# Kernel tuning notes

Measured on AMD Instinct MI355X. Metric: run time of the kernel, lower is better.

## Reference

```python
import jax, jax.numpy as jnp
import numpy as np

B, S, D = 4, 2048, 1024
H = 16
DH = D // H
MLP_DIM = 4096
EPS = 1e-6


def setup_inputs() -> dict:
    key = jax.random.key(0)
    ks = jax.random.split(key, 16)
    sd = lambda fi, fo: (1.0 / np.sqrt(fi))
    return {
        "x": jax.random.normal(ks[0], (B, S, D), jnp.float32),
        "Wq": jax.random.normal(ks[1], (D, D), jnp.float32) * sd(D, D),
        "bq": jnp.zeros((D,), jnp.float32),
        "Wk": jax.random.normal(ks[2], (D, D), jnp.float32) * sd(D, D),
        "bk": jnp.zeros((D,), jnp.float32),
        "Wv": jax.random.normal(ks[3], (D, D), jnp.float32) * sd(D, D),
        "bv": jnp.zeros((D,), jnp.float32),
        "Wo": jax.random.normal(ks[4], (D, D), jnp.float32) * sd(D, D),
        "bo": jnp.zeros((D,), jnp.float32),
        "ln1_g": jnp.ones((D,), jnp.float32),
        "ln1_b": jnp.zeros((D,), jnp.float32),
        "ln2_g": jnp.ones((D,), jnp.float32),
        "ln2_b": jnp.zeros((D,), jnp.float32),
        "W1": jax.random.normal(ks[5], (D, MLP_DIM), jnp.float32) * sd(D, MLP_DIM),
        "b1": jax.random.normal(ks[6], (MLP_DIM,), jnp.float32) * 1e-6,
        "W2": jax.random.normal(ks[7], (MLP_DIM, D), jnp.float32) * sd(MLP_DIM, D),
        "b2": jax.random.normal(ks[8], (D,), jnp.float32) * 1e-6,
    }


def _layernorm(x, g, b):
    mu = jnp.mean(x, axis=-1, keepdims=True)
    var = jnp.mean(jnp.square(x - mu), axis=-1, keepdims=True)
    return (x - mu) * jax.lax.rsqrt(var + EPS) * g + b


def reference(x, Wq, bq, Wk, bk, Wv, bv, Wo, bo,
              ln1_g, ln1_b, ln2_g, ln2_b, W1, b1, W2, b2):
    h = x
    xn = _layernorm(x, ln1_g, ln1_b)
    # Q/K/V: [B,S,D] -> [B,H,S,DH]
    def split_heads(t):
        return t.reshape(B, S, H, DH).transpose(0, 2, 1, 3)
    Q = split_heads(xn @ Wq + bq)
    K = split_heads(xn @ Wk + bk)
    V = split_heads(xn @ Wv + bv)
    scores = jnp.einsum("bhqd,bhkd->bhqk", Q, K) / np.sqrt(DH).astype(np.float32)
    a = jax.nn.softmax(scores, axis=-1)
    r = jnp.einsum("bhqk,bhkd->bhqd", a, V)          # [B,H,S,DH]
    r = r.transpose(0, 2, 1, 3).reshape(B, S, D)      # merge heads
    r = r @ Wo + bo
    x = r + h
    h = x
    xn = _layernorm(x, ln2_g, ln2_b)
    m = jax.nn.gelu(xn @ W1 + b1, approximate=False)
    m = m @ W2 + b2
    return m + h
```

## Files before the change

kernel.cpp:

```cpp
#include <hip/hip_runtime.h>
#include <math.h>

#define B_ 4
#define S_ 2048
#define D_ 1024
#define H_ 16
#define MLP_ 4096
#define MROWS 8192

typedef __attribute__((ext_vector_type(4))) float f32x4;
typedef __attribute__((ext_vector_type(16))) float f32x16;
typedef __attribute__((ext_vector_type(8))) __bf16 bf16x8;
typedef __attribute__((ext_vector_type(4))) __bf16 bf16x4;
typedef __attribute__((ext_vector_type(8))) unsigned short us8;
typedef unsigned short u16;
typedef unsigned int u32;

__device__ __forceinline__ void gload16(const void* g, void* l) {
    __builtin_amdgcn_global_load_lds((const __attribute__((address_space(1))) u32*)g,
                                     (__attribute__((address_space(3))) u32*)l, 16, 0, 0);
}

__device__ __forceinline__ float gelu_f(float v) {
    float p = fmaf(v * v, 0.044715f, 1.0f);
    float e = __builtin_amdgcn_exp2f(v * 2.3022089f * p);
    float r = __builtin_amdgcn_rcpf(e + 1.0f);
    return v - v * r;
}

__global__ __launch_bounds__(256) void ln_bf16_k(const float* __restrict__ x,
                                                 const float* __restrict__ g,
                                                 const float* __restrict__ b,
                                                 u16* __restrict__ y) {
    int row = blockIdx.x;
    int tid = threadIdx.x;
    const float* xr = x + (size_t)row * D_;
    f32x4 v = *(const f32x4*)(xr + tid * 4);
    float s = v.x + v.y + v.z + v.w;
    float ss = v.x * v.x + v.y * v.y + v.z * v.z + v.w * v.w;
    for (int off = 32; off > 0; off >>= 1) {
        s += __shfl_down(s, off, 64);
        ss += __shfl_down(ss, off, 64);
    }
    __shared__ float rs[4], rss[4];
    int lane = tid & 63, wid = tid >> 6;
    if (lane == 0) { rs[wid] = s; rss[wid] = ss; }
    __syncthreads();
    s = rs[0] + rs[1] + rs[2] + rs[3];
    ss = rss[0] + rss[1] + rss[2] + rss[3];
    float mu = s * (1.0f / D_);
    float var = ss * (1.0f / D_) - mu * mu;
    float inv = rsqrtf(var + 1e-6f);
    f32x4 gg = *(const f32x4*)(g + tid * 4);
    f32x4 bb = *(const f32x4*)(b + tid * 4);
    bf16x4 o = {(__bf16)((v.x - mu) * inv * gg.x + bb.x),
                (__bf16)((v.y - mu) * inv * gg.y + bb.y),
                (__bf16)((v.z - mu) * inv * gg.z + bb.z),
                (__bf16)((v.w - mu) * inv * gg.w + bb.w)};
    *(bf16x4*)(y + (size_t)row * D_ + tid * 4) = o;
}

__global__ void pack3_k(const float* __restrict__ a, const float* __restrict__ b,
                        const float* __restrict__ c, float* __restrict__ o) {
    const float* s = blockIdx.x == 0 ? a : (blockIdx.x == 1 ? b : c);
    o[blockIdx.x * 1024 + threadIdx.x] = s[threadIdx.x];
}

__global__ __launch_bounds__(256) void wtrans_k(const float* __restrict__ W,
                                                u16* __restrict__ Wt, int K, int N) {
    __shared__ float T[32][33];
    int tid = threadIdx.x;
    int k0 = blockIdx.y * 32, n0 = blockIdx.x * 32;
    int r = tid >> 3, c4 = (tid & 7) * 4;
    f32x4 v = *(const f32x4*)&W[(size_t)(k0 + r) * N + n0 + c4];
    T[r][c4 + 0] = v.x; T[r][c4 + 1] = v.y; T[r][c4 + 2] = v.z; T[r][c4 + 3] = v.w;
    __syncthreads();
    int n = tid >> 3, kk = (tid & 7) * 4;
    bf16x4 o = {(__bf16)T[kk + 0][n], (__bf16)T[kk + 1][n],
                (__bf16)T[kk + 2][n], (__bf16)T[kk + 3][n]};
    *(bf16x4*)&Wt[(size_t)(n0 + n) * K + k0 + kk] = o;
}

__device__ __forceinline__ int sigma_perm(int s) {
    return (s & 48) | (s & 3) | (((s >> 2) & 1) << 3) | (((s >> 3) & 1) << 2);
}
__global__ __launch_bounds__(256) void vtrans_k(const u16* __restrict__ QKV,
                                                u16* __restrict__ Vt) {
    __shared__ u16 T[64][80];
    int tid = threadIdx.x;
    int s0 = blockIdx.x * 64;
    int bh = blockIdx.y, b = bh >> 4, h = bh & 15;
    int r = tid >> 2, c0 = (tid & 3) * 16;
    const u16* src = QKV + (size_t)(b * S_ + s0 + r) * 3072 + 2048 + h * 64 + c0;
    us8 v0 = *(const us8*)src;
    us8 v1 = *(const us8*)(src + 8);
    *(us8*)&T[r][c0] = v0;
    *(us8*)&T[r][c0 + 8] = v1;
    __syncthreads();
    int dh = tid >> 2, s8 = (tid & 3) * 16;
    us8 o0, o1;
#pragma unroll
    for (int i = 0; i < 8; ++i) {
        o0[i] = T[sigma_perm(s8 + i)][dh];
        o1[i] = T[sigma_perm(s8 + 8 + i)][dh];
    }
    u16* dst = Vt + (size_t)(bh * 64 + dh) * S_ + s0 + s8;
    *(us8*)dst = o0;
    *(us8*)(dst + 8) = o1;
}

template <int EPI>
__global__ __launch_bounds__(256) void gemm_bf16(const u16* __restrict__ A,
                                                 const u16* __restrict__ Wt,
                                                 const float* __restrict__ bias,
                                                 const float* __restrict__ res,
                                                 void* __restrict__ Cout,
                                                 int M, int N, int K) {
    __shared__ u16 As[3][128 * 32];
    __shared__ u16 Bs[3][128 * 32];
    const int tid = threadIdx.x;
    const int lane = tid & 63;
    const int w = tid >> 6;
    const int nwg = gridDim.x * gridDim.y;
    int hw = blockIdx.x + gridDim.x * blockIdx.y;
    int lg = (hw & 7) * (nwg >> 3) + (hw >> 3);
    const int row0 = (lg / gridDim.x) * 128;
    const int col0 = (lg % gridDim.x) * 128;
    const int l15 = lane & 15, l16 = lane >> 4;
    const int wr = w >> 1, wc = w & 1;

    f32x4 acc[4][4];
#pragma unroll
    for (int i = 0; i < 4; ++i)
#pragma unroll
        for (int j = 0; j < 4; ++j) acc[i][j] = (f32x4){0.f, 0.f, 0.f, 0.f};

    const int srow = w * 32 + (lane >> 2);
    const size_t sboff = (size_t)(((lane & 3) ^ ((lane >> 3) & 3)) * 16);
    const char* Ag = (const char*)A + ((size_t)(row0 + srow) * K) * 2 + sboff;
    const char* Bg = (const char*)Wt + ((size_t)(col0 + srow) * K) * 2 + sboff;
    const size_t rstep = (size_t)16 * K * 2;
    const int woff = w * 2048;
    const int T = K >> 5;

#define STAGE(t, bi) do {                                      \
        size_t kb = (size_t)(t) << 6;                          \
        char* asw = (char*)As + (bi) * 8192 + woff;            \
        char* bsw = (char*)Bs + (bi) * 8192 + woff;            \
        gload16(Ag + kb, asw);                                 \
        gload16(Ag + kb + rstep, asw + 1024);                  \
        gload16(Bg + kb, bsw);                                 \
        gload16(Bg + kb + rstep, bsw + 1024);                  \
    } while (0)

    STAGE(0, 0);
    STAGE(1, 1);
    asm volatile("s_waitcnt vmcnt(4)" ::: "memory");
    __builtin_amdgcn_s_barrier();
    __builtin_amdgcn_sched_barrier(0);

    const int ksw = (l16 ^ ((l15 >> 1) & 3)) << 4;
    int bi = 0;
    for (int t = 0; t < T; ++t) {
        if (t + 2 < T) {
            int nb = bi + 2; if (nb >= 3) nb -= 3;
            STAGE(t + 2, nb);
        }
        const char* Ab = (const char*)As + bi * 8192;
        const char* Bb = (const char*)Bs + bi * 8192;
        bf16x8 af[4], bfr[4];
#pragma unroll
        for (int f = 0; f < 4; ++f) {
            af[f] = *(const bf16x8*)(Ab + (size_t)(wr * 64 + f * 16 + l15) * 64 + ksw);
            bfr[f] = *(const bf16x8*)(Bb + (size_t)(wc * 64 + f * 16 + l15) * 64 + ksw);
        }
        __builtin_amdgcn_s_setprio(1);
#pragma unroll
        for (int fi = 0; fi < 4; ++fi)
#pragma unroll
            for (int fj = 0; fj < 4; ++fj)
                acc[fi][fj] = __builtin_amdgcn_mfma_f32_16x16x32_bf16(af[fi], bfr[fj], acc[fi][fj], 0, 0, 0);
        __builtin_amdgcn_s_setprio(0);
        if (t + 2 < T) {
            asm volatile("s_waitcnt vmcnt(4)" ::: "memory");
        } else {
            asm volatile("s_waitcnt vmcnt(0)" ::: "memory");
        }
        __builtin_amdgcn_s_barrier();
        __builtin_amdgcn_sched_barrier(0);
        if (++bi >= 3) bi = 0;
    }
#undef STAGE

    const int rb = row0 + wr * 64 + (l16 << 2);
    const int cb = col0 + wc * 64 + l15;
#pragma unroll
    for (int fi = 0; fi < 4; ++fi)
#pragma unroll
        for (int fj = 0; fj < 4; ++fj) {
            int c = cb + fj * 16;
            float bv = bias[c];
#pragma unroll
            for (int rr = 0; rr < 4; ++rr) {
                int r = rb + fi * 16 + rr;
                float v = acc[fi][fj][rr] + bv;
                if (EPI == 1) v = gelu_f(v);
                if (EPI == 2) {
                    v += res[(size_t)r * N + c];
                    ((float*)Cout)[(size_t)r * N + c] = v;
                } else {
                    ((__bf16*)Cout)[(size_t)r * N + c] = (__bf16)v;
                }
            }
        }
}

__global__ __launch_bounds__(256) void attn_mfma(const u16* __restrict__ QKV,
                                                 const u16* __restrict__ Vt,
                                                 u16* __restrict__ O) {
    __shared__ u16 Ks[2][64 * 64];
    __shared__ u16 Vs[2][64 * 64];
    const int tid = threadIdx.x, lane = tid & 63, w = tid >> 6;
    int hw = blockIdx.x + gridDim.x * blockIdx.y;
    int lg = (hw & 7) * 128 + (hw >> 3);
    const int bh = lg >> 4, b = bh >> 4, h = bh & 15;
    const int q0 = (lg & 15) * 128;
    const int l31 = lane & 31, lh = lane >> 5;

    const u16* Qp = QKV + (size_t)(b * S_ + q0 + w * 32 + l31) * 3072 + h * 64 + lh * 8;
    bf16x8 qf[4];
    qf[0] = *(const bf16x8*)(Qp);
    qf[1] = *(const bf16x8*)(Qp + 16);
    qf[2] = *(const bf16x8*)(Qp + 32);
    qf[3] = *(const bf16x8*)(Qp + 48);

    f32x16 oacc[2];
    f32x16 lacc;
#pragma unroll
    for (int i = 0; i < 16; ++i) { oacc[0][i] = 0.f; oacc[1][i] = 0.f; lacc[i] = 0.f; }
    bf16x8 ones;
#pragma unroll
    for (int j = 0; j < 8; ++j) ones[j] = (__bf16)1.0f;

    const int sr = lane >> 3;
    const size_t soff = (size_t)(((lane & 7) ^ sr) << 4);
    const char* Kg = (const char*)QKV + ((size_t)b * S_ * 3072 + 1024 + h * 64) * 2;
    const char* Vg = (const char*)Vt + (size_t)bh * 64 * S_ * 2;
    const float C2 = 0.18033688011112f;

    const char* kp0 = Kg + (size_t)(w * 16 + sr) * 6144 + soff;
    const char* kp1 = kp0 + 8 * 6144;
    const char* vp0 = Vg + (size_t)(w * 16 + sr) * 4096 + soff;
    const char* vp1 = vp0 + 8 * 4096;
    const size_t KADV = 64 * 6144;
    const size_t VADV = 128;
    char* ksA = (char*)Ks[0] + w * 2048;
    char* ksB = (char*)Ks[1] + w * 2048;
    char* vsA = (char*)Vs[0] + w * 2048;
    char* vsB = (char*)Vs[1] + w * 2048;

    gload16(kp0, ksA); gload16(kp1, ksA + 1024);
    gload16(vp0, vsA); gload16(vp1, vsA + 1024);
    kp0 += KADV; kp1 += KADV; vp0 += VADV; vp1 += VADV;
    __syncthreads();

    for (int kt = 0; kt < S_ / 64; ++kt) {
        const int cur = kt & 1;
        if (kt < S_ / 64 - 1) {
            char* kd = cur ? ksA : ksB;
            char* vd = cur ? vsA : vsB;
            gload16(kp0, kd); gload16(kp1, kd + 1024);
            gload16(vp0, vd); gload16(vp1, vd + 1024);
            kp0 += KADV; kp1 += KADV; vp0 += VADV; vp1 += VADV;
        }

        const char* Kb_ = (const char*)Ks[cur];
        f32x16 sfr[2];
        __builtin_amdgcn_s_setprio(1);
#pragma unroll
        for (int kh = 0; kh < 2; ++kh) {
            int r = kh * 32 + l31;
            int rsw = (r & 7) << 4;
            const char* Kr = Kb_ + r * 128;
            f32x16 t;
#pragma unroll
            for (int i = 0; i < 16; ++i) t[i] = 0.f;
#pragma unroll
            for (int ds = 0; ds < 4; ++ds) {
                bf16x8 kf = *(const bf16x8*)(Kr + ((((ds * 2 + lh) << 4)) ^ rsw));
                t = __builtin_amdgcn_mfma_f32_32x32x16_bf16(kf, qf[ds], t, 0, 0, 0);
            }
            sfr[kh] = t;
        }
        __builtin_amdgcn_s_setprio(0);

        float pv0[16], pv1[16];
#pragma unroll
        for (int i = 0; i < 16; ++i) {
            pv0[i] = __builtin_amdgcn_exp2f(sfr[0][i] * C2);
            pv1[i] = __builtin_amdgcn_exp2f(sfr[1][i] * C2);
        }

        bf16x8 pf[4];
#pragma unroll
        for (int j = 0; j < 8; ++j) {
            pf[0][j] = (__bf16)pv0[j];
            pf[1][j] = (__bf16)pv0[8 + j];
            pf[2][j] = (__bf16)pv1[j];
            pf[3][j] = (__bf16)pv1[8 + j];
        }

        {
            const char* Vb_ = (const char*)Vs[cur];
            __builtin_amdgcn_s_setprio(1);
#pragma unroll
            for (int ks = 0; ks < 4; ++ks)
                lacc = __builtin_amdgcn_mfma_f32_32x32x16_bf16(ones, pf[ks], lacc, 0, 0, 0);
#pragma unroll
            for (int dh = 0; dh < 2; ++dh) {
                int r = dh * 32 + l31;
                int rsw = (r & 7) << 4;
                const char* Vr = Vb_ + r * 128;
#pragma unroll
                for (int ks = 0; ks < 4; ++ks) {
                    bf16x8 vf = *(const bf16x8*)(Vr + ((((ks * 2 + lh) << 4)) ^ rsw));
                    oacc[dh] = __builtin_amdgcn_mfma_f32_32x32x16_bf16(vf, pf[ks], oacc[dh], 0, 0, 0);
                }
            }
            __builtin_amdgcn_s_setprio(0);
        }
        __syncthreads();
    }

    float invl = 1.0f / lacc[0];
    char* Og = (char*)O + ((size_t)(b * S_ + q0 + w * 32 + l31) * 1024 + h * 64) * 2;
#pragma unroll
    for (int dh = 0; dh < 2; ++dh)
#pragma unroll
        for (int t4 = 0; t4 < 4; ++t4) {
            int db = dh * 32 + t4 * 8 + lh * 4;
            bf16x4 ov = {(__bf16)(oacc[dh][t4 * 4] * invl),
                         (__bf16)(oacc[dh][t4 * 4 + 1] * invl),
                         (__bf16)(oacc[dh][t4 * 4 + 2] * invl),
                         (__bf16)(oacc[dh][t4 * 4 + 3] * invl)};
            *(bf16x4*)(Og + db * 2) = ov;
        }
}

extern "C" void kernel_launch(void* const* d_in, const int* in_sizes, int n_in,
                              void* d_out, int out_size, void* d_ws, size_t ws_size,
                              hipStream_t stream) {
    const float* x     = (const float*)d_in[0];
    const float* Wq    = (const float*)d_in[1];
    const float* bq    = (const float*)d_in[2];
    const float* Wk    = (const float*)d_in[3];
    const float* bk    = (const float*)d_in[4];
    const float* Wv    = (const float*)d_in[5];
    const float* bv    = (const float*)d_in[6];
    const float* Wo    = (const float*)d_in[7];
    const float* bo    = (const float*)d_in[8];
    const float* ln1_g = (const float*)d_in[9];
    const float* ln1_b = (const float*)d_in[10];
    const float* ln2_g = (const float*)d_in[11];
    const float* ln2_b = (const float*)d_in[12];
    const float* W1    = (const float*)d_in[13];
    const float* b1    = (const float*)d_in[14];
    const float* W2    = (const float*)d_in[15];
    const float* b2    = (const float*)d_in[16];
    float* out = (float*)d_out;

    const size_t MB = 1ull << 20;
    char* ws = (char*)d_ws;
    u16* QKVb = (u16*)(ws + 0 * MB);
    u16* aout = (u16*)(ws + 48 * MB);
    u16* mid  = (u16*)(ws + 0 * MB);
    float* x2 = (float*)(ws + 64 * MB);
    float* bqkv = (float*)(ws + 64 * MB);
    u16* xn   = (u16*)(ws + 96 * MB);
    u16* Vt   = (u16*)(ws + 96 * MB);
    u16* xn2  = (u16*)(ws + 96 * MB);
    u16* Wqkvt = (u16*)(ws + 112 * MB);
    u16* Wot  = Wqkvt + (size_t)3072 * D_;
    u16* W1t  = (u16*)(ws + 112 * MB);
    u16* W2t  = (u16*)(ws + 120 * MB);

    wtrans_k<<<dim3(32, 32), 256, 0, stream>>>(Wq, Wqkvt, D_, D_);
    wtrans_k<<<dim3(32, 32), 256, 0, stream>>>(Wk, Wqkvt + (size_t)D_ * D_, D_, D_);
    wtrans_k<<<dim3(32, 32), 256, 0, stream>>>(Wv, Wqkvt + (size_t)2 * D_ * D_, D_, D_);
    wtrans_k<<<dim3(32, 32), 256, 0, stream>>>(Wo, Wot, D_, D_);
    wtrans_k<<<dim3(32, 128), 256, 0, stream>>>(W2, W2t, MLP_, D_);
    pack3_k<<<3, 1024, 0, stream>>>(bq, bk, bv, bqkv);

    ln_bf16_k<<<MROWS, 256, 0, stream>>>(x, ln1_g, ln1_b, xn);
    gemm_bf16<0><<<dim3(24, 64), 256, 0, stream>>>(xn, Wqkvt, bqkv, nullptr, QKVb, MROWS, 3072, D_);
    vtrans_k<<<dim3(32, 64), 256, 0, stream>>>(QKVb, Vt);
    attn_mfma<<<dim3(16, 64), 256, 0, stream>>>(QKVb, Vt, aout);
    gemm_bf16<2><<<dim3(8, 64), 256, 0, stream>>>(aout, Wot, bo, x, x2, MROWS, D_, D_);
    wtrans_k<<<dim3(128, 32), 256, 0, stream>>>(W1, W1t, D_, MLP_);
    ln_bf16_k<<<MROWS, 256, 0, stream>>>(x2, ln2_g, ln2_b, xn2);
    gemm_bf16<1><<<dim3(32, 64), 256, 0, stream>>>(xn2, W1t, b1, nullptr, mid, MROWS, MLP_, D_);
    gemm_bf16<2><<<dim3(8, 64), 256, 0, stream>>>(mid, W2t, b2, x2, (void*)out, MROWS, D_, MLP_);
}
```

Measured before the change: 427.2 us.

## Add wide 128x256 GEMM tile with triple buffering; fold softmax scale into Wq

Adds a new gemm_wide kernel that computes 128x256 output tiles with a three-stage LDS ring fed by direct global-to-LDS loads. It is used for the QKV and W1 projections, halving the grid in N and raising the reuse of each A tile. Separately, the softmax scale constant is folded into the Wq weights and bq bias during transposition, which removes a multiply per score inside attention. The wider tile uses more accumulator registers and LDS, which may lower occupancy.

After: 506.8 us. +18.6%, slower.

```diff
diff --git a/kernel.cpp b/kernel.cpp
--- a/kernel.cpp
+++ b/kernel.cpp
@@ -61,13 +61,15 @@
 }
 
 __global__ void pack3_k(const float* __restrict__ a, const float* __restrict__ b,
-                        const float* __restrict__ c, float* __restrict__ o) {
+                        const float* __restrict__ c, float* __restrict__ o, float s0) {
     const float* s = blockIdx.x == 0 ? a : (blockIdx.x == 1 ? b : c);
-    o[blockIdx.x * 1024 + threadIdx.x] = s[threadIdx.x];
+    float sc = blockIdx.x == 0 ? s0 : 1.0f;
+    o[blockIdx.x * 1024 + threadIdx.x] = s[threadIdx.x] * sc;
 }
 
 __global__ __launch_bounds__(256) void wtrans_k(const float* __restrict__ W,
-                                                u16* __restrict__ Wt, int K, int N) {
+                                                u16* __restrict__ Wt, int K, int N,
+                                                float scale) {
     __shared__ float T[32][33];
     int tid = threadIdx.x;
     int k0 = blockIdx.y * 32, n0 = blockIdx.x * 32;
@@ -76,8 +78,8 @@
     T[r][c4 + 0] = v.x; T[r][c4 + 1] = v.y; T[r][c4 + 2] = v.z; T[r][c4 + 3] = v.w;
     __syncthreads();
     int n = tid >> 3, kk = (tid & 7) * 4;
-    bf16x4 o = {(__bf16)T[kk + 0][n], (__bf16)T[kk + 1][n],
-                (__bf16)T[kk + 2][n], (__bf16)T[kk + 3][n]};
+    bf16x4 o = {(__bf16)(T[kk + 0][n] * scale), (__bf16)(T[kk + 1][n] * scale),
+                (__bf16)(T[kk + 2][n] * scale), (__bf16)(T[kk + 3][n] * scale)};
     *(bf16x4*)&Wt[(size_t)(n0 + n) * K + k0 + kk] = o;
 }
 
@@ -215,6 +217,110 @@
         }
 }
 
+template <int EPI>
+__global__ __launch_bounds__(256) void gemm_wide(const u16* __restrict__ A,
+                                                 const u16* __restrict__ Wt,
+                                                 const float* __restrict__ bias,
+                                                 void* __restrict__ Cout,
+                                                 int M, int N, int K) {
+    __shared__ u16 As[3][128 * 32];
+    __shared__ u16 Bs[3][256 * 32];
+    const int tid = threadIdx.x;
+    const int lane = tid & 63;
+    const int w = tid >> 6;
+    const int nwg = gridDim.x * gridDim.y;
+    int hw = blockIdx.x + gridDim.x * blockIdx.y;
+    int lg = (hw & 7) * (nwg >> 3) + (hw >> 3);
+    const int row0 = (lg / gridDim.x) * 128;
+    const int col0 = (lg % gridDim.x) * 256;
+    const int l15 = lane & 15, l16 = lane >> 4;
+    const int wr = w >> 1, wc = w & 1;
+
+    f32x4 acc[4][8];
+#pragma unroll
+    for (int i = 0; i < 4; ++i)
+#pragma unroll
+        for (int j = 0; j < 8; ++j) acc[i][j] = (f32x4){0.f, 0.f, 0.f, 0.f};
+
+    const int srow = lane >> 2;
+    const size_t sboff = (size_t)(((lane & 3) ^ ((lane >> 3) & 3)) * 16);
+    const char* Ag = (const char*)A + ((size_t)(row0 + w * 32 + srow) * K) * 2 + sboff;
+    const char* Bg = (const char*)Wt + ((size_t)(col0 + w * 64 + srow) * K) * 2 + sboff;
+    const size_t rstep = (size_t)16 * K * 2;
+    const int woffA = w * 2048;
+    const int woffB = w * 4096;
+    const int T = K >> 5;
+
+#define STAGEW(t, bi) do {                                     \
+        size_t kb = (size_t)(t) << 6;                          \
+        char* asw = (char*)As + (bi) * 8192 + woffA;           \
+        char* bsw = (char*)Bs + (bi) * 16384 + woffB;          \
+        gload16(Ag + kb, asw);                                 \
+        gload16(Ag + kb + rstep, asw + 1024);                  \
+        gload16(Bg + kb, bsw);                                 \
+        gload16(Bg + kb + rstep, bsw + 1024);                  \
+        gload16(Bg + kb + 2 * rstep, bsw + 2048);              \
+        gload16(Bg + kb + 3 * rstep, bsw + 3072);              \
+    } while (0)
+
+    STAGEW(0, 0);
+    STAGEW(1, 1);
+    asm volatile("s_waitcnt vmcnt(6)" ::: "memory");
+    __builtin_amdgcn_s_barrier();
+    __builtin_amdgcn_sched_barrier(0);
+
+    const int ksw = (l16 ^ ((l15 >> 1) & 3)) << 4;
+    int bi = 0;
+    for (int t = 0; t < T; ++t) {
+        if (t + 2 < T) {
+            int nb = bi + 2; if (nb >= 3) nb -= 3;
+            STAGEW(t + 2, nb);
+        }
+        const char* Ab = (const char*)As + bi * 8192;
+        const char* Bb = (const char*)Bs + bi * 16384;
+        bf16x8 af[4], bfr[8];
+#pragma unroll
+        for (int f = 0; f < 4; ++f)
+            af[f] = *(const bf16x8*)(Ab + (size_t)(wr * 64 + f * 16 + l15) * 64 + ksw);
+#pragma unroll
+        for (int f = 0; f < 8; ++f)
+            bfr[f] = *(const bf16x8*)(Bb + (size_t)(wc * 128 + f * 16 + l15) * 64 + ksw);
+        __builtin_amdgcn_s_setprio(1);
+#pragma unroll
+        for (int fi = 0; fi < 4; ++fi)
+#pragma unroll
+            for (int fj = 0; fj < 8; ++fj)
+                acc[fi][fj] = __builtin_amdgcn_mfma_f32_16x16x32_bf16(af[fi], bfr[fj], acc[fi][fj], 0, 0, 0);
+        __builtin_amdgcn_s_setprio(0);
+        if (t + 2 < T) {
+            asm volatile("s_waitcnt vmcnt(6)" ::: "memory");
+        } else {
+            asm volatile("s_waitcnt vmcnt(0)" ::: "memory");
+        }
+        __builtin_amdgcn_s_barrier();
+        __builtin_amdgcn_sched_barrier(0);
+        if (++bi >= 3) bi = 0;
+    }
+#undef STAGEW
+
+    const int rb = row0 + wr * 64 + (l16 << 2);
+    const int cb = col0 + wc * 128 + l15;
+#pragma unroll
+    for (int fi = 0; fi < 4; ++fi)
+#pragma unroll
+        for (int fj = 0; fj < 8; ++fj) {
+            int c = cb + fj * 16;
+            float bv = bias[c];
+#pragma unroll
+            for (int rr = 0; rr < 4; ++rr) {
+                int r = rb + fi * 16 + rr;
+                float v = acc[fi][fj][rr] + bv;
+                if (EPI == 1) v = gelu_f(v);
+                ((__bf16*)Cout)[(size_t)r * N + c] = (__bf16)v;
+            }
+        }
+}
+
 __global__ __launch_bounds__(256) void attn_mfma(const u16* __restrict__ QKV,
                                                  const u16* __restrict__ Vt,
                                                  u16* __restrict__ O) {
@@ -246,7 +352,6 @@
     const size_t soff = (size_t)(((lane & 7) ^ sr) << 4);
     const char* Kg = (const char*)QKV + ((size_t)b * S_ * 3072 + 1024 + h * 64) * 2;
     const char* Vg = (const char*)Vt + (size_t)bh * 64 * S_ * 2;
-    const float C2 = 0.18033688011112f;
 
     const char* kp0 = Kg + (size_t)(w * 16 + sr) * 6144 + soff;
     const char* kp1 = kp0 + 8 * 6144;
@@ -297,8 +402,8 @@
         float pv0[16], pv1[16];
 #pragma unroll
         for (int i = 0; i < 16; ++i) {
-            pv0[i] = __builtin_amdgcn_exp2f(sfr[0][i] * C2);
-            pv1[i] = __builtin_amdgcn_exp2f(sfr[1][i] * C2);
+            pv0[i] = __builtin_amdgcn_exp2f(sfr[0][i]);
+            pv1[i] = __builtin_amdgcn_exp2f(sfr[1][i]);
         }
 
         bf16x8 pf[4];
@@ -368,6 +473,7 @@
     const float* W2    = (const float*)d_in[15];
     const float* b2    = (const float*)d_in[16];
     float* out = (float*)d_out;
+    const float C2 = 0.18033688011112f;
 
     const size_t MB = 1ull << 20;
     char* ws = (char*)d_ws;
@@ -384,20 +490,20 @@
     u16* W1t  = (u16*)(ws + 112 * MB);
     u16* W2t  = (u16*)(ws + 120 * MB);
 
-    wtrans_k<<<dim3(32, 32), 256, 0, stream>>>(Wq, Wqkvt, D_, D_);
-    wtrans_k<<<dim3(32, 32), 256, 0, stream>>>(Wk, Wqkvt + (size_t)D_ * D_, D_, D_);
-    wtrans_k<<<dim3(32, 32), 256, 0, stream>>>(Wv, Wqkvt + (size_t)2 * D_ * D_, D_, D_);
-    wtrans_k<<<dim3(32, 32), 256, 0, stream>>>(Wo, Wot, D_, D_);
-    wtrans_k<<<dim3(32, 128), 256, 0, stream>>>(W2, W2t, MLP_, D_);
-    pack3_k<<<3, 1024, 0, stream>>>(bq, bk, bv, bqkv);
+    wtrans_k<<<dim3(32, 32), 256, 0, stream>>>(Wq, Wqkvt, D_, D_, C2);
+    wtrans_k<<<dim3(32, 32), 256, 0, stream>>>(Wk, Wqkvt + (size_t)D_ * D_, D_, D_, 1.0f);
+    wtrans_k<<<dim3(32, 32), 256, 0, stream>>>(Wv, Wqkvt + (size_t)2 * D_ * D_, D_, D_, 1.0f);
+    wtrans_k<<<dim3(32, 32), 256, 0, stream>>>(Wo, Wot, D_, D_, 1.0f);
+    wtrans_k<<<dim3(32, 128), 256, 0, stream>>>(W2, W2t, MLP_, D_, 1.0f);
+    pack3_k<<<3, 1024, 0, stream>>>(bq, bk, bv, bqkv, C2);
 
     ln_bf16_k<<<MROWS, 256, 0, stream>>>(x, ln1_g, ln1_b, xn);
-    gemm_bf16<0><<<dim3(24, 64), 256, 0, stream>>>(xn, Wqkvt, bqkv, nullptr, QKVb, MROWS, 3072, D_);
+    gemm_wide<0><<<dim3(12, 64), 256, 0, stream>>>(xn, Wqkvt, bqkv, QKVb, MROWS, 3072, D_);
     vtrans_k<<<dim3(32, 64), 256, 0, stream>>>(QKVb, Vt);
     attn_mfma<<<dim3(16, 64), 256, 0, stream>>>(QKVb, Vt, aout);
     gemm_bf16<2><<<dim3(8, 64), 256, 0, stream>>>(aout, Wot, bo, x, x2, MROWS, D_, D_);
-    wtrans_k<<<dim3(128, 32), 256, 0, stream>>>(W1, W1t, D_, MLP_);
+    wtrans_k<<<dim3(128, 32), 256, 0, stream>>>(W1, W1t, D_, MLP_, 1.0f);
     ln_bf16_k<<<MROWS, 256, 0, stream>>>(x2, ln2_g, ln2_b, xn2);
-    gemm_bf16<1><<<dim3(32, 64), 256, 0, stream>>>(xn2, W1t, b1, nullptr, mid, MROWS, MLP_, D_);
+    gemm_wide<1><<<dim3(16, 64), 256, 0, stream>>>(xn2, W1t, b1, mid, MROWS, MLP_, D_);
     gemm_bf16<2><<<dim3(8, 64), 256, 0, stream>>>(mid, W2t, b2, x2, (void*)out, MROWS, D_, MLP_);
 }
```
